# Kernel tuning notes

Hardware: AMD Instinct MI355X
Metric: run time of the kernel (lower is better)

## Reference

```python
import jax, jax.numpy as jnp
import numpy as np

NUM_EMB = 1024
EMB_DIM = 256
COMMITMENT_COST = 0.25


def setup_inputs() -> dict:
    key = jax.random.key(0)
    k1, k2 = jax.random.split(key)
    inp = jax.random.normal(k1, (64, EMB_DIM, 32, 32), dtype=jnp.float32)  # [B, C, H, W]
    emb_weight = jax.random.uniform(
        k2, (NUM_EMB, EMB_DIM), minval=-1.0 / NUM_EMB, maxval=1.0 / NUM_EMB, dtype=jnp.float32
    )
    return {"inp": inp, "emb_weight": emb_weight}


def reference(inp, emb_weight):
    sg = jax.lax.stop_gradient
    x = jnp.transpose(inp, (0, 2, 3, 1))              # [B, H, W, C]
    flat = x.reshape(-1, EMB_DIM)                      # [N, C]
    d = (jnp.sum(flat * flat, axis=1, keepdims=True)
         + jnp.sum(emb_weight * emb_weight, axis=1)
         - 2.0 * (flat @ emb_weight.T))
    idx = jnp.argmin(d, axis=1)                        # [N]
    encodings = jax.nn.one_hot(idx, NUM_EMB, dtype=jnp.float32)  # [N, K]
    e = emb_weight[idx].reshape(x.shape)               # [B, H, W, C]
    loss = jnp.mean((e - sg(x)) ** 2) + COMMITMENT_COST * jnp.mean((sg(e) - x) ** 2)
    e_ste = x + sg(e - x)                              # straight-through estimator
    avg_probs = jnp.mean(encodings, axis=0)
    perplexity = jnp.exp(-jnp.sum(avg_probs * jnp.log(avg_probs + 1e-10)))
    out = jnp.transpose(e_ste, (0, 3, 1, 2))           # back to [B, C, H, W]
    return loss, out, perplexity, encodings
```

## Files before the change

kernel.cpp:

```cpp
#include <hip/hip_runtime.h>
#include <hip/hip_bf16.h>
#include <math.h>
#include <float.h>

#define BB    64
#define CCH   256
#define KKE   1024
#define HWN   1024
#define NTOT  (BB*HWN)
#define OUT_ELE (BB*CCH*HWN)
#define LOSS_OFF 0
#define OUT_OFF  1
#define PERP_OFF (1 + OUT_ELE)
#define ENC_OFF  (2 + OUT_ELE)

#define WS_IDX    0
#define WS_ANORM  262144
#define WS_HIST   524288
#define WS_BNORM  528384
#define WS_MISC   532480
#define WS_LIST   536576
#define WS_EMBT   798720
#define WS_EHI    1847296
#define WS_ELO    2371584
#define WS_CD1    2895872
#define WS_CK1    4993024
#define WS_CD2    7090176
#define WS_AHI    9187328
#define WS_ALO    42741760

typedef __attribute__((ext_vector_type(4))) float f32x4;
typedef __attribute__((ext_vector_type(2))) float f32x2;
typedef __attribute__((ext_vector_type(8))) short s16x8;

#define TAU 2e-4f
#define RB  8

__device__ __forceinline__ void gload16(const short* g, void* l) {
    __builtin_amdgcn_global_load_lds(
        (const __attribute__((address_space(1))) unsigned int*)g,
        (__attribute__((address_space(3))) unsigned int*)l,
        16, 0, 0);
}

__device__ inline void merge_cand(float& d1, int& k1, float& d2,
                                  float od1, int ok1, float od2) {
    bool w = (od1 < d1) || (od1 == d1 && ok1 < k1);
    float loser_d1 = w ? d1 : od1;
    float winner_d2 = w ? od2 : d2;
    d2 = fminf(winner_d2, loser_d1);
    if (w) { d1 = od1; k1 = ok1; }
}

__global__ __launch_bounds__(256) void prep_split_kernel(const float* __restrict__ emb,
                                                         float* __restrict__ embT,
                                                         float* __restrict__ bnorm,
                                                         short* __restrict__ ehi,
                                                         short* __restrict__ elo,
                                                         unsigned int* __restrict__ hist,
                                                         float* __restrict__ misc,
                                                         const float* __restrict__ inp,
                                                         short* __restrict__ ahi,
                                                         short* __restrict__ alo,
                                                         float* __restrict__ anorm) {
    const int t = threadIdx.x;
    if (blockIdx.x < KKE) {
        const int k = blockIdx.x;
        float v = emb[k*CCH + t];
        embT[(size_t)t*KKE + k] = v;
        __hip_bfloat16 h = __float2bfloat16(v);
        float hf = __bfloat162float(h);
        __hip_bfloat16 l = __float2bfloat16(v - hf);
        const int u  = (t & 31) >> 3;
        const int sw = (k >> 1) & 3;
        size_t eoff = (size_t)(t >> 5)*32768 + (size_t)k*32 + (size_t)((u ^ sw)*8 + (t & 7));
        ehi[eoff] = *(short*)&h;
        elo[eoff] = *(short*)&l;
        double sq = (double)v * (double)v;
        #pragma unroll
        for (int off = 32; off; off >>= 1) sq += __shfl_down(sq, off);
        __shared__ double wred[4];
        const int wave = t >> 6, lane = t & 63;
        if (lane == 0) wred[wave] = sq;
        __syncthreads();
        if (t == 0) bnorm[k] = (float)(wred[0] + wred[1] + wred[2] + wred[3]);
        if (blockIdx.x < 4) hist[blockIdx.x*256 + t] = 0u;
        if (blockIdx.x == 4 && t == 0) { misc[0] = 0.0f; ((int*)misc)[1] = 0; }
    } else {
        __shared__ short th[256*32];
        __shared__ short tl[256*32];
        const int id = blockIdx.x - KKE;
        const int b  = id >> 2;
        const int hw = (id & 3) * 256 + t;
        const int n  = b * HWN + hw;
        const int n0 = n - t;
        const float* src = inp + (size_t)b*CCH*HWN + hw;
        const int sw = (t >> 1) & 3;
        double s = 0.0;
        for (int chunk = 0; chunk < 8; ++chunk) {
            s16x8 hs[4], ls[4];
            #pragma unroll
            for (int cc = 0; cc < 32; ++cc) {
                float v = src[(size_t)(chunk*32 + cc)*HWN];
                s += (double)v * (double)v;
                __hip_bfloat16 h = __float2bfloat16(v);
                float hf = __bfloat162float(h);
                __hip_bfloat16 l = __float2bfloat16(v - hf);
                hs[cc >> 3][cc & 7] = *(short*)&h;
                ls[cc >> 3][cc & 7] = *(short*)&l;
            }
            __syncthreads();
            #pragma unroll
            for (int u = 0; u < 4; ++u) {
                *(s16x8*)&th[t*32 + ((u ^ sw) << 3)] = hs[u];
                *(s16x8*)&tl[t*32 + ((u ^ sw) << 3)] = ls[u];
            }
            __syncthreads();
            const size_t obase = ((size_t)chunk*NTOT + (size_t)n0) * 32;
            #pragma unroll
            for (int i = 0; i < 4; ++i) {
                const int so = i*2048 + t*8;
                *(s16x8*)&ahi[obase + so] = *(const s16x8*)&th[so];
                *(s16x8*)&alo[obase + so] = *(const s16x8*)&tl[so];
            }
        }
        anorm[n] = (float)s;
    }
}

__global__ __launch_bounds__(256, 4) void argmin_mfma(const short* __restrict__ ahi,
                                                      const short* __restrict__ alo,
                                                      const short* __restrict__ ehi,
                                                      const short* __restrict__ elo,
                                                      const float* __restrict__ anorm,
                                                      const float* __restrict__ bnorm,
                                                      float* __restrict__ cd1,
                                                      int* __restrict__ ck1,
                                                      float* __restrict__ cd2) {
    __shared__ short smem[4][4096];

    const int t    = threadIdx.x;
    const int w    = t >> 6;
    const int lane = t & 63;
    const int q    = lane >> 4;
    const int l15  = lane & 15;
    const int L    = blockIdx.x;
    const int bx   = (L & 7) + ((L >> 6) << 3);
    const int by   = (L >> 3) & 7;
    const int n0   = bx * 128;
    const int k0   = by * 128;

    f32x4 acc[2][8];
    #pragma unroll
    for (int i = 0; i < 2; ++i)
        #pragma unroll
        for (int j = 0; j < 8; ++j) acc[i][j] = (f32x4){0.f,0.f,0.f,0.f};

    const int swu = (q ^ ((l15 >> 1) & 3)) << 4;
    const int ra0 = (w*32 + l15)*64 + swu;

    for (int chunk = 0; chunk < 8; ++chunk) {
        __syncthreads();
        {
            const short* as = ahi + (size_t)chunk*2097152 + (size_t)n0*32;
            const short* al = alo + (size_t)chunk*2097152 + (size_t)n0*32;
            const short* bs = ehi + (size_t)chunk*32768  + (size_t)k0*32;
            const short* bl = elo + (size_t)chunk*32768  + (size_t)k0*32;
            #pragma unroll
            for (int i = 0; i < 2; ++i) {
                const size_t so = (size_t)i*2048 + (size_t)t*8;
                const int    lo = i*4096 + w*1024;
                gload16(as + so, (char*)&smem[0][0] + lo);
                gload16(al + so, (char*)&smem[1][0] + lo);
                gload16(bs + so, (char*)&smem[2][0] + lo);
                gload16(bl + so, (char*)&smem[3][0] + lo);
            }
        }
        __syncthreads();
        const char* LAh = (const char*)&smem[0][0];
        const char* LAl = (const char*)&smem[1][0];
        const char* LBh = (const char*)&smem[2][0];
        const char* LBl = (const char*)&smem[3][0];
        s16x8 afh0 = *(const s16x8*)(LAh + ra0);
        s16x8 afh1 = *(const s16x8*)(LAh + ra0 + 1024);
        s16x8 afl0 = *(const s16x8*)(LAl + ra0);
        s16x8 afl1 = *(const s16x8*)(LAl + ra0 + 1024);
        #pragma unroll
        for (int ct = 0; ct < 8; ++ct) {
            const int rb = (ct*16 + l15)*64 + swu;
            s16x8 bh = *(const s16x8*)(LBh + rb);
            s16x8 bl = *(const s16x8*)(LBl + rb);
            acc[0][ct] = __builtin_amdgcn_mfma_f32_16x16x32_bf16(afh0, bh, acc[0][ct], 0, 0, 0);
            acc[0][ct] = __builtin_amdgcn_mfma_f32_16x16x32_bf16(afh0, bl, acc[0][ct], 0, 0, 0);
            acc[0][ct] = __builtin_amdgcn_mfma_f32_16x16x32_bf16(afl0, bh, acc[0][ct], 0, 0, 0);
            acc[1][ct] = __builtin_amdgcn_mfma_f32_16x16x32_bf16(afh1, bh, acc[1][ct], 0, 0, 0);
            acc[1][ct] = __builtin_amdgcn_mfma_f32_16x16x32_bf16(afh1, bl, acc[1][ct], 0, 0, 0);
            acc[1][ct] = __builtin_amdgcn_mfma_f32_16x16x32_bf16(afl1, bh, acc[1][ct], 0, 0, 0);
        }
    }

    float bnv[8];
    #pragma unroll
    for (int ct = 0; ct < 8; ++ct) bnv[ct] = bnorm[k0 + ct*16 + l15];

    #pragma unroll
    for (int rg = 0; rg < 2; ++rg) {
        #pragma unroll
        for (int reg = 0; reg < 4; ++reg) {
            const int n = n0 + w*32 + rg*16 + q*4 + reg;
            const float a = anorm[n];
            float d1 = FLT_MAX, d2 = FLT_MAX; int k1 = 0;
            #pragma unroll
            for (int ct = 0; ct < 8; ++ct) {
                float s = a + bnv[ct];
                float d = s - 2.0f * acc[rg][ct][reg];
                int   k = k0 + ct*16 + l15;
                if (d < d1 || (d == d1 && k < k1)) { d2 = d1; d1 = d; k1 = k; }
                else d2 = fminf(d2, d);
            }
            #pragma unroll
            for (int off = 1; off < 16; off <<= 1) {
                float od1 = __shfl_xor(d1, off);
                int   ok1 = __shfl_xor(k1, off);
                float od2 = __shfl_xor(d2, off);
                merge_cand(d1, k1, d2, od1, ok1, od2);
            }
            if (l15 == 0) {
                const size_t o = (size_t)by*NTOT + n;
                cd1[o] = d1; ck1[o] = k1; cd2[o] = d2;
            }
        }
    }
}

__global__ __launch_bounds__(256) void reduce_kernel(const float* __restrict__ cd1,
                                                     const int* __restrict__ ck1,
                                                     const float* __restrict__ cd2,
                                                     int* __restrict__ idx,
                                                     int* __restrict__ list,
                                                     int* __restrict__ counter) {
    const int n = blockIdx.x*256 + threadIdx.x;
    float d1 = cd1[n]; int k1 = ck1[n]; float d2 = cd2[n];
    #pragma unroll
    for (int kb = 1; kb < 8; ++kb) {
        const size_t o = (size_t)kb*NTOT + n;
        merge_cand(d1, k1, d2, cd1[o], ck1[o], cd2[o]);
    }
    idx[n] = k1;
    if (d2 - d1 < TAU) {
        int p = atomicAdd(counter, 1);
        list[p] = n;
    }
}

__global__ __launch_bounds__(256) void rescore_kernel(const float* __restrict__ inp,
                                                      const float* __restrict__ embT,
                                                      const float* __restrict__ anorm,
                                                      const float* __restrict__ bnorm,
                                                      const int* __restrict__ list,
                                                      const int* __restrict__ counter,
                                                      int* __restrict__ idx) {
    __shared__ float xs[RB][256];
    __shared__ float wd[RB][4];
    __shared__ int   wk[RB][4];
    __shared__ int   ls[RB];
    const int t = threadIdx.x;
    const int wave = t >> 6, lane = t & 63;
    const int cnt = *counter;
    const int ngrp = (cnt + RB - 1) / RB;
    float bn[4];
    #pragma unroll
    for (int kk = 0; kk < 4; ++kk) bn[kk] = bnorm[kk*256 + t];

    for (int g = blockIdx.x; g < ngrp; g += gridDim.x) {
        const int base = g * RB;
        const int m = min(RB, cnt - base);
        __syncthreads();
        if (t < RB) ls[t] = list[base + ((t < m) ? t : 0)];
        __syncthreads();
        #pragma unroll
        for (int j = 0; j < RB; ++j) {
            const int n = ls[j];
            xs[j][t] = inp[(size_t)(n >> 10)*CCH*HWN + (size_t)t*HWN + (n & 1023)];
        }
        __syncthreads();
        float dots[RB][4];
        #pragma unroll
        for (int j = 0; j < RB; ++j)
            #pragma unroll
            for (int kk = 0; kk < 4; ++kk) dots[j][kk] = 0.f;
        #pragma unroll 4
        for (int c = 0; c < CCH; ++c) {
            const float* row = embT + (size_t)c*KKE + t;
            const float e0 = row[0], e1 = row[256], e2 = row[512], e3 = row[768];
            #pragma unroll
            for (int j = 0; j < RB; ++j) {
                const float xc = xs[j][c];
                dots[j][0] += xc * e0;
                dots[j][1] += xc * e1;
                dots[j][2] += xc * e2;
                dots[j][3] += xc * e3;
            }
        }
        #pragma unroll
        for (int j = 0; j < RB; ++j) {
            const float a = anorm[ls[j]];
            float bd = FLT_MAX; int bk = 0;
            #pragma unroll
            for (int kk = 0; kk < 4; ++kk) {
                const int k = kk*256 + t;
                float s = a + bn[kk];
                float d = s - 2.0f * dots[j][kk];
                if (d < bd || (d == bd && k < bk)) { bd = d; bk = k; }
            }
            #pragma unroll
            for (int off = 1; off < 64; off <<= 1) {
                float od = __shfl_xor(bd, off);
                int   ok = __shfl_xor(bk, off);
                if (od < bd || (od == bd && ok < bk)) { bd = od; bk = ok; }
            }
            if (lane == 0) { wd[j][wave] = bd; wk[j][wave] = bk; }
        }
        __syncthreads();
        if (t < m) {
            float bd = wd[t][0]; int bk = wk[t][0];
            #pragma unroll
            for (int wv = 1; wv < 4; ++wv) {
                float od = wd[t][wv]; int ok = wk[t][wv];
                if (od < bd || (od == bd && ok < bk)) { bd = od; bk = ok; }
            }
            idx[ls[t]] = bk;
        }
    }
}

#define ENC_BLK 4096
#define OL_BLK  4096
__global__ __launch_bounds__(256) void tail_kernel(const float* __restrict__ inp,
                                                   const float* __restrict__ embT,
                                                   const int* __restrict__ idx,
                                                   float* __restrict__ enc,
                                                   float* __restrict__ out,
                                                   unsigned int* __restrict__ hist,
                                                   float* __restrict__ lossacc) {
    const int t = threadIdx.x;
    if (blockIdx.x < ENC_BLK) {
        const int n0 = blockIdx.x * 16;
        int kr[16];
        #pragma unroll
        for (int r4 = 0; r4 < 4; ++r4) {
            int4 kv = *(const int4*)&idx[n0 + r4*4];
            kr[r4*4+0] = kv.x; kr[r4*4+1] = kv.y; kr[r4*4+2] = kv.z; kr[r4*4+3] = kv.w;
        }
        const int j4 = t*4 + 2;
        #pragma unroll 8
        for (int r = 0; r < 16; ++r) {
            const int k = kr[r];
            float* row = enc + (size_t)(n0 + r) * KKE;
            if (t < 255) {
                f32x4 v = {0.f,0.f,0.f,0.f};
                if (k == j4)     v.x = 1.f;
                if (k == j4 + 1) v.y = 1.f;
                if (k == j4 + 2) v.z = 1.f;
                if (k == j4 + 3) v.w = 1.f;
                __builtin_nontemporal_store(v, (f32x4*)&row[j4]);
            } else {
                f32x2 h  = {0.f,0.f}, tl = {0.f,0.f};
                if (k == 0)    h.x  = 1.f;
                if (k == 1)    h.y  = 1.f;
                if (k == 1022) tl.x = 1.f;
                if (k == 1023) tl.y = 1.f;
                __builtin_nontemporal_store(h,  (f32x2*)&row[0]);
                __builtin_nontemporal_store(tl, (f32x2*)&row[1022]);
            }
            if (t == 0) atomicAdd(&hist[k], 1u);
        }
    } else {
        const size_t stride = (size_t)OL_BLK * 256;
        float lsum = 0.0f;
        for (size_t m = (size_t)(blockIdx.x - ENC_BLK) * 256 + t; m < (size_t)OUT_ELE; m += stride) {
            int hw = (int)(m & 1023);
            int c  = (int)((m >> 10) & 255);
            int b  = (int)(m >> 18);
            int k  = idx[b*HWN + hw];
            float e = embT[(size_t)c*KKE + k];
            float x = inp[m];
            __builtin_nontemporal_store(e, &out[m]);
            float df = e - x;
            lsum += df * df;
        }
        #pragma unroll
        for (int off = 32; off; off >>= 1) lsum += __shfl_down(lsum, off);
        __shared__ float wred[4];
        const int wave = t >> 6, lane = t & 63;
        if (lane == 0) wred[wave] = lsum;
        __syncthreads();
        if (t == 0) atomicAdd(lossacc, wred[0] + wred[1] + wred[2] + wred[3]);
    }
}

__global__ __launch_bounds__(1024) void final_kernel(const unsigned int* __restrict__ hist,
                                                     const float* __restrict__ lossacc,
                                                     float* __restrict__ d_out) {
    const int t = threadIdx.x;
    float p = (float)hist[t] * (1.0f / 65536.0f);
    float v = p * logf(p + 1e-10f);
    #pragma unroll
    for (int off = 32; off; off >>= 1) v += __shfl_down(v, off);
    __shared__ float wred[16];
    const int wave = t >> 6, lane = t & 63;
    if (lane == 0) wred[wave] = v;
    __syncthreads();
    if (t == 0) {
        float s = 0.0f;
        #pragma unroll
        for (int i = 0; i < 16; ++i) s += wred[i];
        d_out[PERP_OFF] = expf(-s);
        d_out[LOSS_OFF] = 1.25f * (*lossacc) * (1.0f / (float)OUT_ELE);
    }
}

extern "C" void kernel_launch(void* const* d_in, const int* in_sizes, int n_in,
                              void* d_out, int out_size, void* d_ws, size_t ws_size,
                              hipStream_t stream) {
    (void)in_sizes; (void)n_in; (void)out_size; (void)ws_size;
    const float* inp = (const float*)d_in[0];
    const float* emb = (const float*)d_in[1];
    float* out = (float*)d_out;
    char* ws = (char*)d_ws;
    int*          idx     = (int*)(ws + WS_IDX);
    float*        anorm   = (float*)(ws + WS_ANORM);
    unsigned int* hist    = (unsigned int*)(ws + WS_HIST);
    float*        bnorm   = (float*)(ws + WS_BNORM);
    float*        misc    = (float*)(ws + WS_MISC);
    int*          list    = (int*)(ws + WS_LIST);
    float*        embT    = (float*)(ws + WS_EMBT);
    short*        ehi     = (short*)(ws + WS_EHI);
    short*        elo     = (short*)(ws + WS_ELO);
    float*        cd1     = (float*)(ws + WS_CD1);
    int*          ck1     = (int*)(ws + WS_CK1);
    float*        cd2     = (float*)(ws + WS_CD2);
    short*        ahi     = (short*)(ws + WS_AHI);
    short*        alo     = (short*)(ws + WS_ALO);
    int*          counter = ((int*)misc) + 1;

    prep_split_kernel<<<dim3(KKE + 256), dim3(256), 0, stream>>>(emb, embT, bnorm, ehi, elo,
                                                                 hist, misc, inp, ahi, alo, anorm);
    argmin_mfma<<<dim3(4096), dim3(256), 0, stream>>>(ahi, alo, ehi, elo, anorm, bnorm, cd1, ck1, cd2);
    reduce_kernel<<<dim3(256), dim3(256), 0, stream>>>(cd1, ck1, cd2, idx, list, counter);
    rescore_kernel<<<dim3(512), dim3(256), 0, stream>>>(inp, embT, anorm, bnorm, list, counter, idx);
    tail_kernel<<<dim3(ENC_BLK + OL_BLK), dim3(256), 0, stream>>>(inp, embT, idx, out + ENC_OFF, out + OUT_OFF, hist, misc);
    final_kernel<<<dim3(1), dim3(1024), 0, stream>>>(hist, misc, out);
}
```

Before: 647.5 us.

## Keep A rows in registers, loop over all codebook tiles, fuse candidate reduction

The argmin kernel now gives each block 128 rows across the full 1024-entry codebook. The A fragments for all 8 channel chunks are held in registers, and B tiles are streamed through a double-buffered LDS stage. The running best and second-best candidates stay in registers, so the separate reduce kernel and the cd1/ck1/cd2 intermediate writes are removed, and A is read once instead of once per codebook tile. The cost is much higher register pressure (64 VGPRs of A plus accumulators), and only 512 blocks are launched, which lowers occupancy and parallelism.

New measurement: 693.8 us. 7.2% more time.

```diff
diff --git a/kernel.cpp b/kernel.cpp
--- a/kernel.cpp
+++ b/kernel.cpp
@@ -23,9 +23,6 @@
 #define WS_EMBT   798720
 #define WS_EHI    1847296
 #define WS_ELO    2371584
-#define WS_CD1    2895872
-#define WS_CK1    4993024
-#define WS_CD2    7090176
 #define WS_AHI    9187328
 #define WS_ALO    42741760
 
@@ -128,96 +125,122 @@
     }
 }
 
-__global__ __launch_bounds__(256, 4) void argmin_mfma(const short* __restrict__ ahi,
-                                                      const short* __restrict__ alo,
-                                                      const short* __restrict__ ehi,
-                                                      const short* __restrict__ elo,
-                                                      const float* __restrict__ anorm,
-                                                      const float* __restrict__ bnorm,
-                                                      float* __restrict__ cd1,
-                                                      int* __restrict__ ck1,
-                                                      float* __restrict__ cd2) {
-    __shared__ short smem[4][4096];
+__global__ __launch_bounds__(256) void argmin_mfma(const short* __restrict__ ahi,
+                                                   const short* __restrict__ alo,
+                                                   const short* __restrict__ ehi,
+                                                   const short* __restrict__ elo,
+                                                   const float* __restrict__ anorm,
+                                                   const float* __restrict__ bnorm,
+                                                   int* __restrict__ idx,
+                                                   int* __restrict__ list,
+                                                   int* __restrict__ counter) {
+    __shared__ short smem[2][2][4096];
 
     const int t    = threadIdx.x;
     const int w    = t >> 6;
     const int lane = t & 63;
     const int q    = lane >> 4;
     const int l15  = lane & 15;
-    const int L    = blockIdx.x;
-    const int bx   = (L & 7) + ((L >> 6) << 3);
-    const int by   = (L >> 3) & 7;
-    const int n0   = bx * 128;
-    const int k0   = by * 128;
-
-    f32x4 acc[2][8];
-    #pragma unroll
-    for (int i = 0; i < 2; ++i)
-        #pragma unroll
-        for (int j = 0; j < 8; ++j) acc[i][j] = (f32x4){0.f,0.f,0.f,0.f};
+    const int n0   = blockIdx.x * 128;
 
     const int swu = (q ^ ((l15 >> 1) & 3)) << 4;
     const int ra0 = (w*32 + l15)*64 + swu;
 
-    for (int chunk = 0; chunk < 8; ++chunk) {
-        __syncthreads();
-        {
-            const short* as = ahi + (size_t)chunk*2097152 + (size_t)n0*32;
-            const short* al = alo + (size_t)chunk*2097152 + (size_t)n0*32;
-            const short* bs = ehi + (size_t)chunk*32768  + (size_t)k0*32;
-            const short* bl = elo + (size_t)chunk*32768  + (size_t)k0*32;
-            #pragma unroll
-            for (int i = 0; i < 2; ++i) {
-                const size_t so = (size_t)i*2048 + (size_t)t*8;
-                const int    lo = i*4096 + w*1024;
-                gload16(as + so, (char*)&smem[0][0] + lo);
-                gload16(al + so, (char*)&smem[1][0] + lo);
-                gload16(bs + so, (char*)&smem[2][0] + lo);
-                gload16(bl + so, (char*)&smem[3][0] + lo);
-            }
-        }
-        __syncthreads();
-        const char* LAh = (const char*)&smem[0][0];
-        const char* LAl = (const char*)&smem[1][0];
-        const char* LBh = (const char*)&smem[2][0];
-        const char* LBl = (const char*)&smem[3][0];
-        s16x8 afh0 = *(const s16x8*)(LAh + ra0);
-        s16x8 afh1 = *(const s16x8*)(LAh + ra0 + 1024);
-        s16x8 afl0 = *(const s16x8*)(LAl + ra0);
-        s16x8 afl1 = *(const s16x8*)(LAl + ra0 + 1024);
-        #pragma unroll
-        for (int ct = 0; ct < 8; ++ct) {
-            const int rb = (ct*16 + l15)*64 + swu;
-            s16x8 bh = *(const s16x8*)(LBh + rb);
-            s16x8 bl = *(const s16x8*)(LBl + rb);
-            acc[0][ct] = __builtin_amdgcn_mfma_f32_16x16x32_bf16(afh0, bh, acc[0][ct], 0, 0, 0);
-            acc[0][ct] = __builtin_amdgcn_mfma_f32_16x16x32_bf16(afh0, bl, acc[0][ct], 0, 0, 0);
-            acc[0][ct] = __builtin_amdgcn_mfma_f32_16x16x32_bf16(afl0, bh, acc[0][ct], 0, 0, 0);
-            acc[1][ct] = __builtin_amdgcn_mfma_f32_16x16x32_bf16(afh1, bh, acc[1][ct], 0, 0, 0);
-            acc[1][ct] = __builtin_amdgcn_mfma_f32_16x16x32_bf16(afh1, bl, acc[1][ct], 0, 0, 0);
-            acc[1][ct] = __builtin_amdgcn_mfma_f32_16x16x32_bf16(afl1, bh, acc[1][ct], 0, 0, 0);
-        }
-    }
-
-    float bnv[8];
-    #pragma unroll
-    for (int ct = 0; ct < 8; ++ct) bnv[ct] = bnorm[k0 + ct*16 + l15];
+    s16x8 Ah[8][2], Al[8][2];
+    #pragma unroll
+    for (int ch = 0; ch < 8; ++ch) {
+        const char* pah = (const char*)ahi + (size_t)ch*4194304 + (size_t)n0*64;
+        const char* pal = (const char*)alo + (size_t)ch*4194304 + (size_t)n0*64;
+        Ah[ch][0] = *(const s16x8*)(pah + ra0);
+        Ah[ch][1] = *(const s16x8*)(pah + ra0 + 1024);
+        Al[ch][0] = *(const s16x8*)(pal + ra0);
+        Al[ch][1] = *(const s16x8*)(pal + ra0 + 1024);
+    }
+
+    float areg[2][4];
+    #pragma unroll
+    for (int rg = 0; rg < 2; ++rg)
+        #pragma unroll
+        for (int reg = 0; reg < 4; ++reg)
+            areg[rg][reg] = anorm[n0 + w*32 + rg*16 + q*4 + reg];
+
+    float rd1[2][4], rd2[2][4]; int rk1[2][4];
+    #pragma unroll
+    for (int rg = 0; rg < 2; ++rg)
+        #pragma unroll
+        for (int reg = 0; reg < 4; ++reg) { rd1[rg][reg] = FLT_MAX; rd2[rg][reg] = FLT_MAX; rk1[rg][reg] = 0; }
+
+    auto stage = [&](int buf, int kt, int ch) {
+        const short* bs = ehi + (size_t)ch*32768 + (size_t)kt*4096;
+        const short* bl = elo + (size_t)ch*32768 + (size_t)kt*4096;
+        #pragma unroll
+        for (int i = 0; i < 2; ++i) {
+            const size_t so = (size_t)i*2048 + (size_t)t*8;
+            const int    lo = i*4096 + w*1024;
+            gload16(bs + so, (char*)&smem[buf][0][0] + lo);
+            gload16(bl + so, (char*)&smem[buf][1][0] + lo);
+        }
+    };
+
+    stage(0, 0, 0);
+    int cur = 0;
+    for (int kt = 0; kt < 8; ++kt) {
+        f32x4 acc[2][8];
+        #pragma unroll
+        for (int i = 0; i < 2; ++i)
+            #pragma unroll
+            for (int j = 0; j < 8; ++j) acc[i][j] = (f32x4){0.f,0.f,0.f,0.f};
+
+        #pragma unroll
+        for (int ch = 0; ch < 8; ++ch) {
+            __syncthreads();
+            const int snext = kt*8 + ch + 1;
+            if (snext < 64) stage(cur ^ 1, snext >> 3, snext & 7);
+            const char* LBh = (const char*)&smem[cur][0][0];
+            const char* LBl = (const char*)&smem[cur][1][0];
+            #pragma unroll
+            for (int ct = 0; ct < 8; ++ct) {
+                const int rb = (ct*16 + l15)*64 + swu;
+                s16x8 bh = *(const s16x8*)(LBh + rb);
+                s16x8 bl = *(const s16x8*)(LBl + rb);
+                acc[0][ct] = __builtin_amdgcn_mfma_f32_16x16x32_bf16(Ah[ch][0], bh, acc[0][ct], 0, 0, 0);
+                acc[0][ct] = __builtin_amdgcn_mfma_f32_16x16x32_bf16(Ah[ch][0], bl, acc[0][ct], 0, 0, 0);
+                acc[0][ct] = __builtin_amdgcn_mfma_f32_16x16x32_bf16(Al[ch][0], bh, acc[0][ct], 0, 0, 0);
+                acc[1][ct] = __builtin_amdgcn_mfma_f32_16x16x32_bf16(Ah[ch][1], bh, acc[1][ct], 0, 0, 0);
+                acc[1][ct] = __builtin_amdgcn_mfma_f32_16x16x32_bf16(Ah[ch][1], bl, acc[1][ct], 0, 0, 0);
+                acc[1][ct] = __builtin_amdgcn_mfma_f32_16x16x32_bf16(Al[ch][1], bh, acc[1][ct], 0, 0, 0);
+            }
+            cur ^= 1;
+        }
+
+        const int k0 = kt * 128;
+        float bnv[8];
+        #pragma unroll
+        for (int ct = 0; ct < 8; ++ct) bnv[ct] = bnorm[k0 + ct*16 + l15];
+        #pragma unroll
+        for (int rg = 0; rg < 2; ++rg) {
+            #pragma unroll
+            for (int reg = 0; reg < 4; ++reg) {
+                const float a = areg[rg][reg];
+                float d1 = rd1[rg][reg], d2 = rd2[rg][reg]; int k1 = rk1[rg][reg];
+                #pragma unroll
+                for (int ct = 0; ct < 8; ++ct) {
+                    float s = a + bnv[ct];
+                    float d = s - 2.0f * acc[rg][ct][reg];
+                    int   k = k0 + ct*16 + l15;
+                    if (d < d1 || (d == d1 && k < k1)) { d2 = d1; d1 = d; k1 = k; }
+                    else d2 = fminf(d2, d);
+                }
+                rd1[rg][reg] = d1; rd2[rg][reg] = d2; rk1[rg][reg] = k1;
+            }
+        }
+    }
 
     #pragma unroll
     for (int rg = 0; rg < 2; ++rg) {
         #pragma unroll
         for (int reg = 0; reg < 4; ++reg) {
-            const int n = n0 + w*32 + rg*16 + q*4 + reg;
-            const float a = anorm[n];
-            float d1 = FLT_MAX, d2 = FLT_MAX; int k1 = 0;
-            #pragma unroll
-            for (int ct = 0; ct < 8; ++ct) {
-                float s = a + bnv[ct];
-                float d = s - 2.0f * acc[rg][ct][reg];
-                int   k = k0 + ct*16 + l15;
-                if (d < d1 || (d == d1 && k < k1)) { d2 = d1; d1 = d; k1 = k; }
-                else d2 = fminf(d2, d);
-            }
+            float d1 = rd1[rg][reg], d2 = rd2[rg][reg]; int k1 = rk1[rg][reg];
             #pragma unroll
             for (int off = 1; off < 16; off <<= 1) {
                 float od1 = __shfl_xor(d1, off);
@@ -226,30 +249,14 @@
                 merge_cand(d1, k1, d2, od1, ok1, od2);
             }
             if (l15 == 0) {
-                const size_t o = (size_t)by*NTOT + n;
-                cd1[o] = d1; ck1[o] = k1; cd2[o] = d2;
-            }
-        }
-    }
-}
-
-__global__ __launch_bounds__(256) void reduce_kernel(const float* __restrict__ cd1,
-                                                     const int* __restrict__ ck1,
-                                                     const float* __restrict__ cd2,
-                                                     int* __restrict__ idx,
-                                                     int* __restrict__ list,
-                                                     int* __restrict__ counter) {
-    const int n = blockIdx.x*256 + threadIdx.x;
-    float d1 = cd1[n]; int k1 = ck1[n]; float d2 = cd2[n];
-    #pragma unroll
-    for (int kb = 1; kb < 8; ++kb) {
-        const size_t o = (size_t)kb*NTOT + n;
-        merge_cand(d1, k1, d2, cd1[o], ck1[o], cd2[o]);
-    }
-    idx[n] = k1;
-    if (d2 - d1 < TAU) {
-        int p = atomicAdd(counter, 1);
-        list[p] = n;
+                const int n = n0 + w*32 + rg*16 + q*4 + reg;
+                idx[n] = k1;
+                if (d2 - d1 < TAU) {
+                    int p = atomicAdd(counter, 1);
+                    list[p] = n;
+                }
+            }
+        }
     }
 }
 
@@ -437,17 +444,13 @@
     float*        embT    = (float*)(ws + WS_EMBT);
     short*        ehi     = (short*)(ws + WS_EHI);
     short*        elo     = (short*)(ws + WS_ELO);
-    float*        cd1     = (float*)(ws + WS_CD1);
-    int*          ck1     = (int*)(ws + WS_CK1);
-    float*        cd2     = (float*)(ws + WS_CD2);
     short*        ahi     = (short*)(ws + WS_AHI);
     short*        alo     = (short*)(ws + WS_ALO);
     int*          counter = ((int*)misc) + 1;
 
     prep_split_kernel<<<dim3(KKE + 256), dim3(256), 0, stream>>>(emb, embT, bnorm, ehi, elo,
                                                                  hist, misc, inp, ahi, alo, anorm);
-    argmin_mfma<<<dim3(4096), dim3(256), 0, stream>>>(ahi, alo, ehi, elo, anorm, bnorm, cd1, ck1, cd2);
-    reduce_kernel<<<dim3(256), dim3(256), 0, stream>>>(cd1, ck1, cd2, idx, list, counter);
+    argmin_mfma<<<dim3(512), dim3(256), 0, stream>>>(ahi, alo, ehi, elo, anorm, bnorm, idx, list, counter);
     rescore_kernel<<<dim3(512), dim3(256), 0, stream>>>(inp, embT, anorm, bnorm, list, counter, idx);
     tail_kernel<<<dim3(ENC_BLK + OL_BLK), dim3(256), 0, stream>>>(inp, embT, idx, out + ENC_OFF, out + OUT_OFF, hist, misc);
     final_kernel<<<dim3(1), dim3(1024), 0, stream>>>(hist, misc, out);
```
